# Optimization experiments

Hardware: AMD Instinct MI355X
Metric: run time of the kernel (lower is better)

## Reference

```python
import jax, jax.numpy as jnp
import numpy as np

B, S, C = 4, 2048, 2048
D = C // 4  # head dim = 512

def setup_inputs() -> dict:
    key = jax.random.key(0)
    k1, k2, k3, k4, k5 = jax.random.split(key, 5)
    scale = 1.0 / np.sqrt(C)
    return {
        "x": jax.random.normal(k1, (B, S, C), dtype=jnp.float32),
        "Wqkv": jax.random.normal(k2, (3 * D, C), dtype=jnp.float32) * scale,
        "bqkv": jax.random.normal(k3, (3 * D,), dtype=jnp.float32) * 0.01,
        "Wo": jax.random.normal(k4, (C, D), dtype=jnp.float32) * (1.0 / np.sqrt(D)),
        "bo": jax.random.normal(k5, (C,), dtype=jnp.float32) * 0.01,
    }

def reference(x, Wqkv, bqkv, Wo, bo):
    Bx, Sx, Cx = x.shape
    d = Cx // 4
    # fused QKV projection: [B,S,3d] -> split into q,k,v each [B,S,d]
    qkv = jnp.einsum('bsc,oc->bso', x, Wqkv) + bqkv
    qkv = qkv.reshape(Bx, Sx, 3, d)
    q, k, v = qkv[:, :, 0], qkv[:, :, 1], qkv[:, :, 2]
    # scaled dot-product attention (full [B,S,S] scores, as in original)
    attn = jnp.einsum('bqd,bkd->bqk', q, k) / jnp.sqrt(jnp.asarray(d, x.dtype))
    attn = jax.nn.softmax(attn, axis=-1)
    ctx = jnp.einsum('bqk,bkd->bqd', attn, v)
    # output projection d -> C
    return jnp.einsum('bsd,od->bso', ctx, Wo) + bo
```

## Files before the change

kernel.cpp:

```cpp
#include <hip/hip_runtime.h>
#include <math.h>


typedef __bf16 bf16;
typedef bf16 bf16x8 __attribute__((ext_vector_type(8)));
typedef bf16 bf16x4 __attribute__((ext_vector_type(4)));
typedef float f32x4 __attribute__((ext_vector_type(4)));

#define BB 4
#define SS 2048
#define CC 2048
#define DD 512
#define ND3 1536
#define MM 8192

typedef const __attribute__((address_space(1))) unsigned int g_u32;
typedef __attribute__((address_space(3))) unsigned int l_u32;

__device__ __forceinline__ void gl_lds16(const bf16* g, bf16* l) {
    __builtin_amdgcn_global_load_lds((g_u32*)g, (l_u32*)l, 16, 0, 0);
}

#define VMW(n) asm volatile("s_waitcnt vmcnt(" #n ")" ::: "memory")
#define LKW0   asm volatile("s_waitcnt lgkmcnt(0)" ::: "memory")
#define BAR    __builtin_amdgcn_s_barrier()

#define N4_X   (MM * CC / 4)
#define N4_WQ  (ND3 * CC / 4)
#define N4_WO  (CC * DD / 4)
#define N4_RS  (MM / 4)
#define N4_TOT (N4_X + N4_WQ + N4_WO + N4_RS)

__global__ __launch_bounds__(256) void prep(const float* __restrict__ x,
                                            const float* __restrict__ Wqkv,
                                            const float* __restrict__ Wo,
                                            bf16* __restrict__ xb,
                                            bf16* __restrict__ wqkvb,
                                            bf16* __restrict__ wob,
                                            float* __restrict__ rsum) {
    int i = blockIdx.x * 256 + threadIdx.x;
    const int stride = gridDim.x * 256;
    for (; i < N4_TOT; i += stride) {
        if (i < N4_X + N4_WQ + N4_WO) {
            const float* src; bf16* dst; int j = i;
            if (j < N4_X)                { src = x;    dst = xb; }
            else if (j < N4_X + N4_WQ)   { src = Wqkv; dst = wqkvb; j -= N4_X; }
            else                         { src = Wo;   dst = wob;   j -= N4_X + N4_WQ; }
            float4 v = ((const float4*)src)[j];
            bf16x4 o;
            o[0] = (bf16)v.x; o[1] = (bf16)v.y; o[2] = (bf16)v.z; o[3] = (bf16)v.w;
            ((bf16x4*)dst)[j] = o;
        } else {
            int j = i - (N4_X + N4_WQ + N4_WO);
            ((float4*)rsum)[j] = float4{0.f, 0.f, 0.f, 0.f};
        }
    }
}

#define SLOT_E 16384
#define CH_B   8192

template <bool OUT_BF16, int EPI>
__device__ __forceinline__ void gemm256_body(const bf16* __restrict__ A,
                                             const bf16* __restrict__ Bm,
                                             const float* __restrict__ bias,
                                             float* __restrict__ rowsum,
                                             bf16* __restrict__ vTp,
                                             void* __restrict__ Cv,
                                             int K, int lda, int ldb, int ldc,
                                             long ab, long bb, long cb,
                                             float scale) {
    extern __shared__ bf16 lds[];
    A  += (size_t)blockIdx.z * ab;
    Bm += (size_t)blockIdx.z * bb;
    const int m0 = blockIdx.y * 256, n0 = blockIdx.x * 256;
    const int t = threadIdx.x, lane = t & 63, w = t >> 6;
    const int wm = (w >> 2) * 128, wn = (w & 3) * 64;
    const int cl = lane & 15, q = lane >> 4;
    const int swzr = (q ^ ((cl >> 1) & 3)) * 8;
    const int srow = t >> 2;
    const int swz  = (t & 3) ^ ((t >> 3) & 3);
    const bf16* pa = A  + (size_t)(m0 + srow) * lda + swz * 8;
    const bf16* pb = Bm + (size_t)(n0 + srow) * ldb + swz * 8;
    bf16* lw = lds + w * 512;

    f32x4 acc[8][4] = {};
    const int NC = K >> 5;

    auto STAGE = [&](int j) {
        bf16* s = lw + (j & 1) * SLOT_E;
        const bf16* ga = pa + j * 32;
        const bf16* gb = pb + j * 32;
        gl_lds16(ga,                     s);
        gl_lds16(ga + (size_t)128 * lda, s + 4096);
        gl_lds16(gb,                     s + CH_B);
        gl_lds16(gb + (size_t)128 * ldb, s + CH_B + 4096);
    };
    auto FRAGS = [&](int j, bf16x8 (&af)[8], bf16x8 (&bfr)[4]) {
        const bf16* sa = lds + (j & 1) * SLOT_E + (wm + cl) * 32 + swzr;
        const bf16* sb = lds + (j & 1) * SLOT_E + CH_B + (wn + cl) * 32 + swzr;
#pragma unroll
        for (int i = 0; i < 8; i++)  af[i]  = *(const bf16x8*)(sa + i * 512);
#pragma unroll
        for (int jj = 0; jj < 4; jj++) bfr[jj] = *(const bf16x8*)(sb + jj * 512);
    };
    auto MFMAS = [&](bf16x8 (&af)[8], bf16x8 (&bfr)[4]) {
        __builtin_amdgcn_s_setprio(1);
#pragma unroll
        for (int i = 0; i < 8; i++)
#pragma unroll
            for (int jj = 0; jj < 4; jj++)
                acc[i][jj] = __builtin_amdgcn_mfma_f32_16x16x32_bf16(
                                 af[i], bfr[jj], acc[i][jj], 0, 0, 0);
        __builtin_amdgcn_s_setprio(0);
    };

    STAGE(0); STAGE(1);
    VMW(4); BAR;

    for (int j = 0; j < NC - 2; ++j) {
        bf16x8 af[8], bfr[4];
        FRAGS(j, af, bfr);
        MFMAS(af, bfr);
        LKW0; BAR;
        STAGE(j + 2);
        VMW(4); BAR;
    }
    {   bf16x8 af[8], bfr[4];
        FRAGS(NC - 2, af, bfr); MFMAS(af, bfr);
        VMW(0); BAR;
    }
    {   bf16x8 af[8], bfr[4];
        FRAGS(NC - 1, af, bfr); MFMAS(af, bfr);
    }

    if constexpr (EPI == 4) {
        float cs[4] = {0.f, 0.f, 0.f, 0.f};
#pragma unroll
        for (int i = 0; i < 8; i++)
#pragma unroll
            for (int jj = 0; jj < 4; jj++) {
                int col = n0 + wn + jj * 16 + cl;
                int row = m0 + wm + i * 16 + q * 4;
                bf16x4 o;
#pragma unroll
                for (int r = 0; r < 4; r++) {
                    float e = __expf(acc[i][jj][r] * scale);
                    cs[jj] += e;
                    o[r] = (bf16)e;
                }
                *(bf16x4*)&((bf16*)Cv)[(size_t)blockIdx.z * cb + (size_t)col * ldc + row] = o;
            }
#pragma unroll
        for (int jj = 0; jj < 4; jj++) {
            cs[jj] += __shfl_xor(cs[jj], 16, 64);
            cs[jj] += __shfl_xor(cs[jj], 32, 64);
        }
        if (q == 0) {
#pragma unroll
            for (int jj = 0; jj < 4; jj++)
                atomicAdd(&rowsum[(size_t)blockIdx.z * SS + n0 + wn + jj * 16 + cl], cs[jj]);
        }
        return;
    }

    const bool v_block = (EPI == 3) && (n0 >= 1024);
#pragma unroll
    for (int i = 0; i < 8; i++) {
#pragma unroll
        for (int jj = 0; jj < 4; jj++) {
            int col = n0 + wn + jj * 16 + cl;
            float bvv = bias ? bias[col] : 0.0f;
            if (v_block) {
                int row = m0 + wm + i * 16 + q * 4;
                int b = row >> 11, s = row & 2047;
                bf16x4 o;
#pragma unroll
                for (int r = 0; r < 4; r++) o[r] = (bf16)(acc[i][jj][r] * scale + bvv);
                *(bf16x4*)&vTp[((size_t)b * DD + (col - 1024)) * SS + s] = o;
            } else {
#pragma unroll
                for (int r = 0; r < 4; r++) {
                    int row = m0 + wm + i * 16 + q * 4 + r;
                    float val = acc[i][jj][r] * scale + bvv;
                    if (OUT_BF16)
                        ((bf16*)Cv)[(size_t)blockIdx.z * cb + (size_t)row * ldc + col] = (bf16)val;
                    else
                        ((float*)Cv)[(size_t)blockIdx.z * cb + (size_t)row * ldc + col] = val;
                }
            }
        }
    }
}

__global__ __launch_bounds__(256) void k_pv(const bf16* __restrict__ A,
        const bf16* __restrict__ Bm, float* __restrict__ rowsum,
        bf16* __restrict__ Cv, int K, int lda, int ldb, int ldc,
        long ab, long bb, long cb) {
    __shared__ bf16 As[128 * 64];
    __shared__ bf16 Bs[64 * 64];
    A += (size_t)blockIdx.z * ab;
    Bm += (size_t)blockIdx.z * bb;
    const int m0 = blockIdx.y * 128, n0 = blockIdx.x * 64;
    const int t = threadIdx.x, lane = t & 63, w = t >> 6;
    const int wm = w * 32;
    const int q = lane >> 4, cl = lane & 15;
    const int srow = lane >> 3;
    const int sblk = (lane & 7) ^ srow;
    const int scol = sblk * 8;
    const bf16* pa = A + (size_t)(m0 + w * 32 + srow) * lda + scol;
    const bf16* pb = Bm + (size_t)(n0 + w * 16 + srow) * ldb + scol;
    bf16* lA = As + (w * 32) * 64;
    bf16* lB = Bs + (w * 16) * 64;
    const int rblk0 = (q ^ (cl & 7)) * 8;
    const int rblk1 = ((4 + q) ^ (cl & 7)) * 8;

    f32x4 acc[2][4] = {};
    for (int k0 = 0; k0 < K; k0 += 64) {
#pragma unroll
        for (int n = 0; n < 4; n++)
            gl_lds16(pa + k0 + (size_t)(n * 8) * lda, lA + n * 8 * 64);
#pragma unroll
        for (int n = 0; n < 2; n++)
            gl_lds16(pb + k0 + (size_t)(n * 8) * ldb, lB + n * 8 * 64);
        __syncthreads();
#pragma unroll
        for (int h = 0; h < 2; h++) {
            const int rb = h ? rblk1 : rblk0;
            bf16x8 af[2], bfr[4];
#pragma unroll
            for (int i = 0; i < 2; i++)
                af[i] = *(const bf16x8*)&As[(wm + i * 16 + cl) * 64 + rb];
#pragma unroll
            for (int j = 0; j < 4; j++)
                bfr[j] = *(const bf16x8*)&Bs[(j * 16 + cl) * 64 + rb];
#pragma unroll
            for (int i = 0; i < 2; i++)
#pragma unroll
                for (int j = 0; j < 4; j++)
                    acc[i][j] = __builtin_amdgcn_mfma_f32_16x16x32_bf16(af[i], bfr[j], acc[i][j], 0, 0, 0);
        }
        __syncthreads();
    }

    float inv[2][4];
#pragma unroll
    for (int i = 0; i < 2; i++)
#pragma unroll
        for (int r = 0; r < 4; r++)
            inv[i][r] = 1.0f / rowsum[(size_t)blockIdx.z * SS + m0 + wm + i * 16 + q * 4 + r];
#pragma unroll
    for (int i = 0; i < 2; i++)
#pragma unroll
        for (int j = 0; j < 4; j++) {
            int col = n0 + j * 16 + cl;
#pragma unroll
            for (int r = 0; r < 4; r++) {
                int row = m0 + wm + i * 16 + q * 4 + r;
                Cv[(size_t)blockIdx.z * cb + (size_t)row * ldc + col] =
                    (bf16)(acc[i][j][r] * inv[i][r]);
            }
        }
}

__global__ __launch_bounds__(512, 2) void k_qkv(const bf16* A, const bf16* Bm,
        const float* bias, bf16* vTp, void* Cv, int K, int lda, int ldb, int ldc,
        float scale) {
    gemm256_body<true, 3>(A, Bm, bias, nullptr, vTp, Cv, K, lda, ldb, ldc, 0, 0, 0, scale);
}
__global__ __launch_bounds__(512, 2) void k_score(const bf16* A, const bf16* Bm,
        float* rowsum, void* Cv, int K, int lda, int ldb, int ldc,
        long ab, long bb, long cb, float scale) {
    gemm256_body<true, 4>(A, Bm, nullptr, rowsum, nullptr, Cv, K, lda, ldb, ldc, ab, bb, cb, scale);
}
__global__ __launch_bounds__(512, 2) void k_out(const bf16* A, const bf16* Bm,
        const float* bias, void* Cv, int K, int lda, int ldb, int ldc,
        float scale) {
    gemm256_body<false, 0>(A, Bm, bias, nullptr, nullptr, Cv, K, lda, ldb, ldc, 0, 0, 0, scale);
}

extern "C" void kernel_launch(void* const* d_in, const int* in_sizes, int n_in,
                              void* d_out, int out_size, void* d_ws, size_t ws_size,
                              hipStream_t stream) {
    const float* x    = (const float*)d_in[0];
    const float* Wqkv = (const float*)d_in[1];
    const float* bqkv = (const float*)d_in[2];
    const float* Wo   = (const float*)d_in[3];
    const float* bo   = (const float*)d_in[4];
    float* out = (float*)d_out;

    char* ws = (char*)d_ws;
    size_t off = 0;
    bf16* xb    = (bf16*)(ws + off); off += (size_t)MM * CC * 2;
    bf16* wqkvb = (bf16*)(ws + off); off += (size_t)ND3 * CC * 2;
    bf16* wob   = (bf16*)(ws + off); off += (size_t)CC * DD * 2;
    bf16* qkvb  = (bf16*)(ws + off); off += (size_t)MM * ND3 * 2;
    bf16* vT    = (bf16*)(ws + off); off += (size_t)BB * DD * SS * 2;
    bf16* expS  = (bf16*)(ws + off); off += (size_t)BB * SS * SS * 2;
    bf16* ctxb  = (bf16*)(ws + off); off += (size_t)MM * DD * 2;
    float* rsum = (float*)(ws + off); off += (size_t)MM * 4;

    static int lds_attr_set = 0;
    if (!lds_attr_set) {
        hipFuncSetAttribute((const void*)k_qkv,
                            hipFuncAttributeMaxDynamicSharedMemorySize, 65536);
        hipFuncSetAttribute((const void*)k_score,
                            hipFuncAttributeMaxDynamicSharedMemorySize, 65536);
        hipFuncSetAttribute((const void*)k_out,
                            hipFuncAttributeMaxDynamicSharedMemorySize, 65536);
        lds_attr_set = 1;
    }

    prep<<<2048, 256, 0, stream>>>(x, Wqkv, Wo, xb, wqkvb, wob, rsum);

    k_qkv<<<dim3(ND3 / 256, MM / 256, 1), 512, 65536, stream>>>(
        xb, wqkvb, bqkv, vT, qkvb, CC, CC, CC, ND3, 1.0f);

    k_score<<<dim3(SS / 256, SS / 256, BB), 512, 65536, stream>>>(
        qkvb + 512 , qkvb , rsum, expS,
        DD, ND3, ND3, SS,
        (long)SS * ND3, (long)SS * ND3, (long)SS * SS,
        0.044194173824159216f );

    k_pv<<<dim3(DD / 64, SS / 128, BB), 256, 0, stream>>>(
        expS, vT, rsum, ctxb,
        SS, SS, SS, DD,
        (long)SS * SS, (long)DD * SS, (long)SS * DD);

    k_out<<<dim3(CC / 256, MM / 256, 1), 512, 65536, stream>>>(
        ctxb, wob, bo, out, DD, DD, DD, CC, 1.0f);

    (void)in_sizes; (void)n_in; (void)out_size; (void)ws_size;
}
```

Measured before the change: 297.0 us.

## Deepen GEMM LDS pipeline to four stages, add XCD block swizzle, transpose PV

Grows the shared 256x256 GEMM body from double to quad buffering, 128 KB of LDS. Each next stage is issued before the MFMAs of the current one, which drops the lgkmcnt wait and one barrier per iteration. A block-index remap spreads adjacent tiles across the eight XCDs for better L2 locality, and is applied to every GEMM. The PV kernel now computes the transposed product (vT x expS), which makes normalisation per-column and allows vectorised bf16x4 stores. With 128 KB of LDS per block, only one block fits per CU, which risks lower occupancy.

```diff
diff --git a/kernel.cpp b/kernel.cpp
--- a/kernel.cpp
+++ b/kernel.cpp
@@ -22,8 +22,18 @@
 }
 
 #define VMW(n) asm volatile("s_waitcnt vmcnt(" #n ")" ::: "memory")
-#define LKW0   asm volatile("s_waitcnt lgkmcnt(0)" ::: "memory")
 #define BAR    __builtin_amdgcn_s_barrier()
+
+__device__ __forceinline__ void xcd_swz(int& bx, int& by, int& bz) {
+    const int gx = gridDim.x, gy = gridDim.y;
+    const int nwg = gx * gy * gridDim.z;
+    const int d = (blockIdx.z * gy + blockIdx.y) * gx + blockIdx.x;
+    const int s = (d & 7) * (nwg >> 3) + (d >> 3);
+    bx = s % gx;
+    const int t2 = s / gx;
+    by = t2 % gy;
+    bz = t2 / gy;
+}
 
 #define N4_X   (MM * CC / 4)
 #define N4_WQ  (ND3 * CC / 4)
@@ -71,9 +81,11 @@
                                              long ab, long bb, long cb,
                                              float scale) {
     extern __shared__ bf16 lds[];
-    A  += (size_t)blockIdx.z * ab;
-    Bm += (size_t)blockIdx.z * bb;
-    const int m0 = blockIdx.y * 256, n0 = blockIdx.x * 256;
+    int bx, by, bz;
+    xcd_swz(bx, by, bz);
+    A  += (size_t)bz * ab;
+    Bm += (size_t)bz * bb;
+    const int m0 = by * 256, n0 = bx * 256;
     const int t = threadIdx.x, lane = t & 63, w = t >> 6;
     const int wm = (w >> 2) * 128, wn = (w & 3) * 64;
     const int cl = lane & 15, q = lane >> 4;
@@ -88,7 +100,7 @@
     const int NC = K >> 5;
 
     auto STAGE = [&](int j) {
-        bf16* s = lw + (j & 1) * SLOT_E;
+        bf16* s = lw + (j & 3) * SLOT_E;
         const bf16* ga = pa + j * 32;
         const bf16* gb = pb + j * 32;
         gl_lds16(ga,                     s);
@@ -97,8 +109,8 @@
         gl_lds16(gb + (size_t)128 * ldb, s + CH_B + 4096);
     };
     auto FRAGS = [&](int j, bf16x8 (&af)[8], bf16x8 (&bfr)[4]) {
-        const bf16* sa = lds + (j & 1) * SLOT_E + (wm + cl) * 32 + swzr;
-        const bf16* sb = lds + (j & 1) * SLOT_E + CH_B + (wn + cl) * 32 + swzr;
+        const bf16* sa = lds + (j & 3) * SLOT_E + (wm + cl) * 32 + swzr;
+        const bf16* sb = lds + (j & 3) * SLOT_E + CH_B + (wn + cl) * 32 + swzr;
 #pragma unroll
         for (int i = 0; i < 8; i++)  af[i]  = *(const bf16x8*)(sa + i * 512);
 #pragma unroll
@@ -115,15 +127,18 @@
         __builtin_amdgcn_s_setprio(0);
     };
 
-    STAGE(0); STAGE(1);
-    VMW(4); BAR;
-
-    for (int j = 0; j < NC - 2; ++j) {
+    STAGE(0); STAGE(1); STAGE(2);
+    VMW(8); BAR;
+
+    for (int j = 0; j < NC - 3; ++j) {
         bf16x8 af[8], bfr[4];
         FRAGS(j, af, bfr);
+        STAGE(j + 3);
         MFMAS(af, bfr);
-        LKW0; BAR;
-        STAGE(j + 2);
+        VMW(8); BAR;
+    }
+    {   bf16x8 af[8], bfr[4];
+        FRAGS(NC - 3, af, bfr); MFMAS(af, bfr);
         VMW(4); BAR;
     }
     {   bf16x8 af[8], bfr[4];
@@ -149,7 +164,7 @@
                     cs[jj] += e;
                     o[r] = (bf16)e;
                 }
-                *(bf16x4*)&((bf16*)Cv)[(size_t)blockIdx.z * cb + (size_t)col * ldc + row] = o;
+                *(bf16x4*)&((bf16*)Cv)[(size_t)bz * cb + (size_t)col * ldc + row] = o;
             }
 #pragma unroll
         for (int jj = 0; jj < 4; jj++) {
@@ -159,7 +174,7 @@
         if (q == 0) {
 #pragma unroll
             for (int jj = 0; jj < 4; jj++)
-                atomicAdd(&rowsum[(size_t)blockIdx.z * SS + n0 + wn + jj * 16 + cl], cs[jj]);
+                atomicAdd(&rowsum[(size_t)bz * SS + n0 + wn + jj * 16 + cl], cs[jj]);
         }
         return;
     }
@@ -184,9 +199,9 @@
                     int row = m0 + wm + i * 16 + q * 4 + r;
                     float val = acc[i][jj][r] * scale + bvv;
                     if (OUT_BF16)
-                        ((bf16*)Cv)[(size_t)blockIdx.z * cb + (size_t)row * ldc + col] = (bf16)val;
+                        ((bf16*)Cv)[(size_t)bz * cb + (size_t)row * ldc + col] = (bf16)val;
                     else
-                        ((float*)Cv)[(size_t)blockIdx.z * cb + (size_t)row * ldc + col] = val;
+                        ((float*)Cv)[(size_t)bz * cb + (size_t)row * ldc + col] = val;
                 }
             }
         }
@@ -199,11 +214,13 @@
         long ab, long bb, long cb) {
     __shared__ bf16 As[128 * 64];
     __shared__ bf16 Bs[64 * 64];
-    A += (size_t)blockIdx.z * ab;
-    Bm += (size_t)blockIdx.z * bb;
-    const int m0 = blockIdx.y * 128, n0 = blockIdx.x * 64;
+    int bx, by, bz;
+    xcd_swz(bx, by, bz);
+    A += (size_t)bz * ab;
+    Bm += (size_t)bz * bb;
+    const int m0 = by * 128, n0 = bx * 64;
     const int t = threadIdx.x, lane = t & 63, w = t >> 6;
-    const int wm = w * 32;
+    const int wm = w * 32, wn = 0;
     const int q = lane >> 4, cl = lane & 15;
     const int srow = lane >> 3;
     const int sblk = (lane & 7) ^ srow;
@@ -233,7 +250,7 @@
                 af[i] = *(const bf16x8*)&As[(wm + i * 16 + cl) * 64 + rb];
 #pragma unroll
             for (int j = 0; j < 4; j++)
-                bfr[j] = *(const bf16x8*)&Bs[(j * 16 + cl) * 64 + rb];
+                bfr[j] = *(const bf16x8*)&Bs[(wn + j * 16 + cl) * 64 + rb];
 #pragma unroll
             for (int i = 0; i < 2; i++)
 #pragma unroll
@@ -243,23 +260,20 @@
         __syncthreads();
     }
 
-    float inv[2][4];
+    float inv[4];
+#pragma unroll
+    for (int j = 0; j < 4; j++)
+        inv[j] = 1.0f / rowsum[(size_t)bz * SS + n0 + wn + j * 16 + cl];
 #pragma unroll
     for (int i = 0; i < 2; i++)
 #pragma unroll
-        for (int r = 0; r < 4; r++)
-            inv[i][r] = 1.0f / rowsum[(size_t)blockIdx.z * SS + m0 + wm + i * 16 + q * 4 + r];
-#pragma unroll
-    for (int i = 0; i < 2; i++)
-#pragma unroll
         for (int j = 0; j < 4; j++) {
-            int col = n0 + j * 16 + cl;
-#pragma unroll
-            for (int r = 0; r < 4; r++) {
-                int row = m0 + wm + i * 16 + q * 4 + r;
-                Cv[(size_t)blockIdx.z * cb + (size_t)row * ldc + col] =
-                    (bf16)(acc[i][j][r] * inv[i][r]);
-            }
+            int col = n0 + wn + j * 16 + cl;
+            int row = m0 + wm + i * 16 + q * 4;
+            bf16x4 o;
+#pragma unroll
+            for (int r = 0; r < 4; r++) o[r] = (bf16)(acc[i][j][r] * inv[j]);
+            *(bf16x4*)&Cv[(size_t)bz * cb + (size_t)col * ldc + row] = o;
         }
 }
 
@@ -303,31 +317,31 @@
     static int lds_attr_set = 0;
     if (!lds_attr_set) {
         hipFuncSetAttribute((const void*)k_qkv,
-                            hipFuncAttributeMaxDynamicSharedMemorySize, 65536);
+                            hipFuncAttributeMaxDynamicSharedMemorySize, 131072);
         hipFuncSetAttribute((const void*)k_score,
-                            hipFuncAttributeMaxDynamicSharedMemorySize, 65536);
+                            hipFuncAttributeMaxDynamicSharedMemorySize, 131072);
         hipFuncSetAttribute((const void*)k_out,
-                            hipFuncAttributeMaxDynamicSharedMemorySize, 65536);
+                            hipFuncAttributeMaxDynamicSharedMemorySize, 131072);
         lds_attr_set = 1;
     }
 
     prep<<<2048, 256, 0, stream>>>(x, Wqkv, Wo, xb, wqkvb, wob, rsum);
 
-    k_qkv<<<dim3(ND3 / 256, MM / 256, 1), 512, 65536, stream>>>(
+    k_qkv<<<dim3(ND3 / 256, MM / 256, 1), 512, 131072, stream>>>(
         xb, wqkvb, bqkv, vT, qkvb, CC, CC, CC, ND3, 1.0f);
 
-    k_score<<<dim3(SS / 256, SS / 256, BB), 512, 65536, stream>>>(
+    k_score<<<dim3(SS / 256, SS / 256, BB), 512, 131072, stream>>>(
         qkvb + 512 , qkvb , rsum, expS,
         DD, ND3, ND3, SS,
         (long)SS * ND3, (long)SS * ND3, (long)SS * SS,
         0.044194173824159216f );
 
-    k_pv<<<dim3(DD / 64, SS / 128, BB), 256, 0, stream>>>(
-        expS, vT, rsum, ctxb,
+    k_pv<<<dim3(SS / 64, DD / 128, BB), 256, 0, stream>>>(
+        vT, expS, rsum, ctxb,
         SS, SS, SS, DD,
-        (long)SS * SS, (long)DD * SS, (long)SS * DD);
-
-    k_out<<<dim3(CC / 256, MM / 256, 1), 512, 65536, stream>>>(
+        (long)DD * SS, (long)SS * SS, (long)SS * DD);
+
+    k_out<<<dim3(CC / 256, MM / 256, 1), 512, 131072, stream>>>(
         ctxb, wob, bo, out, DD, DD, DD, CC, 1.0f);
 
     (void)in_sizes; (void)n_in; (void)out_size; (void)ws_size;
```

Result: faster. 273.4 us (-8.0%).
